# Performance work log

Measured on AMD Instinct MI355X. Metric: run time of the kernel, lower is better.

## Reference

```python
import jax, jax.numpy as jnp
import numpy as np

D_MODEL = 2048
N_HEADS = 16
N_KV = 4
D_HEAD = D_MODEL // N_HEADS  # 128
N_REP = N_HEADS // N_KV      # 4
ROPE_BASE = 1000000.0


def _rope_tables(T, d_head, dtype):
    # inv_freq = (1/base)^(2i/d) for i in [0, d/2)
    i = jnp.arange(d_head // 2, dtype=jnp.float32)
    inv_freq = (1.0 / ROPE_BASE) ** (2.0 * i / d_head)
    theta = jnp.arange(T, dtype=jnp.float32)[:, None] * inv_freq[None, :]  # [T, d/2]
    theta = jnp.concatenate([theta, theta], axis=-1)                        # [T, d]
    return jnp.sin(theta).astype(dtype), jnp.cos(theta).astype(dtype)


def _apply_rope(x, sin, cos):
    # x: [B, h, T, d]; sin/cos: [T, d]
    x1, x2 = jnp.split(x, 2, axis=-1)
    rot = jnp.concatenate([-x2, x1], axis=-1)
    return cos[None, None] * x + sin[None, None] * rot


def setup_inputs() -> dict:
    key = jax.random.key(0)
    ks = jax.random.split(key, 9)
    B, T = 2, 2048
    s_in = 1.0 / np.sqrt(D_MODEL)
    return {
        "x": jax.random.normal(ks[0], (B, T, D_MODEL), jnp.float32),
        "wq": jax.random.normal(ks[1], (D_MODEL, N_HEADS * D_HEAD), jnp.float32) * s_in,
        "bq": jax.random.normal(ks[2], (N_HEADS * D_HEAD,), jnp.float32) * 0.02,
        "wk": jax.random.normal(ks[3], (D_MODEL, N_KV * D_HEAD), jnp.float32) * s_in,
        "bk": jax.random.normal(ks[4], (N_KV * D_HEAD,), jnp.float32) * 0.02,
        "wv": jax.random.normal(ks[5], (D_MODEL, N_KV * D_HEAD), jnp.float32) * s_in,
        "bv": jax.random.normal(ks[6], (N_KV * D_HEAD,), jnp.float32) * 0.02,
        "wo": jax.random.normal(ks[7], (D_MODEL, D_MODEL), jnp.float32) * s_in,
    }


def reference(x, wq, bq, wk, bk, wv, bv, wo):
    B, T, C = x.shape
    sin, cos = _rope_tables(T, D_HEAD, x.dtype)

    q = (x @ wq + bq).reshape(B, T, N_HEADS, D_HEAD).transpose(0, 2, 1, 3)  # [B,H,T,d]
    k = (x @ wk + bk).reshape(B, T, N_KV, D_HEAD).transpose(0, 2, 1, 3)     # [B,KV,T,d]
    v = (x @ wv + bv).reshape(B, T, N_KV, D_HEAD).transpose(0, 2, 1, 3)     # [B,KV,T,d]

    q = _apply_rope(q, sin, cos)
    k = _apply_rope(k, sin, cos)

    # GQA: group query heads as [B, KV, rep, T, d] to broadcast against k/v
    qg = q.reshape(B, N_KV, N_REP, T, D_HEAD)
    scale = 1.0 / jnp.sqrt(jnp.asarray(D_HEAD, x.dtype))
    scores = jnp.einsum('bkrqd,bksd->bkrqs', qg, k) * scale  # [B,KV,rep,T,S]

    causal = jnp.tril(jnp.ones((T, T), dtype=bool))
    neg = jnp.asarray(jnp.finfo(x.dtype).min, x.dtype)
    scores = jnp.where(causal[None, None, None], scores, neg)
    p = jax.nn.softmax(scores, axis=-1)

    out = jnp.einsum('bkrqs,bksd->bkrqd', p, v)               # [B,KV,rep,T,d]
    out = out.reshape(B, N_HEADS, T, D_HEAD).transpose(0, 2, 1, 3).reshape(B, T, C)
    return out @ wo, k, v
```

## Files before the change

### kernel.cpp

```cpp
#include <hip/hip_runtime.h>
#include <hip/hip_bf16.h>
#include <math.h>

#define BB 2
#define TT 2048
#define DMODEL 2048
#define NH 16
#define NKV 4
#define DH 128
#define NQKV 3072
#define MM (BB*TT)

typedef unsigned short u16;
typedef unsigned int u32;

typedef __bf16 bf16x8 __attribute__((ext_vector_type(8)));
typedef __bf16 bf16x4 __attribute__((ext_vector_type(4)));
typedef short short4v __attribute__((ext_vector_type(4)));
typedef float f32x4 __attribute__((ext_vector_type(4)));

__device__ __forceinline__ u16 f2b(float f) {
  union { float f; u32 u; } v; v.f = f;
  u32 r = v.u + 0x7fffu + ((v.u >> 16) & 1u);
  return (u16)(r >> 16);
}
__device__ __forceinline__ float b2f(u16 h) {
  union { u32 u; float f; } v; v.u = ((u32)h) << 16;
  return v.f;
}
__device__ __forceinline__ u32 pack2bf(float x, float y) {
  union { float f; u32 u; } a, b; a.f = x; b.f = y;
  return ((a.u + 0x8000u) >> 16) | ((b.u + 0x8000u) & 0xffff0000u);
}

__device__ __forceinline__ void gload16(const void* g, void* l) {
  __builtin_amdgcn_global_load_lds(
      (const __attribute__((address_space(1))) unsigned int*)g,
      (__attribute__((address_space(3))) unsigned int*)l, 16, 0, 0);
}

__device__ __forceinline__ float fast_exp2(float x) {
#if __has_builtin(__builtin_amdgcn_exp2f)
  return __builtin_amdgcn_exp2f(x);
#else
  return __expf(x * 0.6931471805599453f);
#endif
}

__device__ __forceinline__ f32x4 mfma16(bf16x4 a, bf16x4 b, f32x4 c) {
#if __has_builtin(__builtin_amdgcn_mfma_f32_16x16x16bf16_1k)
  union { bf16x4 b; short4v s; } ua, ub;
  ua.b = a; ub.b = b;
  return __builtin_amdgcn_mfma_f32_16x16x16bf16_1k(ua.s, ub.s, c, 0, 0, 0);
#elif __has_builtin(__builtin_amdgcn_mfma_f32_16x16x16_bf16)
  return __builtin_amdgcn_mfma_f32_16x16x16_bf16(a, b, c, 0, 0, 0);
#else
  asm volatile("v_mfma_f32_16x16x16_bf16 %0, %1, %2, %0"
               : "+v"(c) : "v"(a), "v"(b));
  return c;
#endif
}

__global__ void cvt_x_kernel(const float* __restrict__ x, u16* __restrict__ xb, int n4) {
  int i = blockIdx.x * 256 + threadIdx.x;
  if (i < n4) {
    float4 v = ((const float4*)x)[i];
    u32 lo = (u32)f2b(v.x) | ((u32)f2b(v.y) << 16);
    u32 hi = (u32)f2b(v.z) | ((u32)f2b(v.w) << 16);
    uint2 r; r.x = lo; r.y = hi;
    ((uint2*)xb)[i] = r;
  }
}

__global__ void bias_cat_kernel(const float* __restrict__ bq, const float* __restrict__ bk,
                                const float* __restrict__ bv, float* __restrict__ bc) {
  int i = blockIdx.x * 256 + threadIdx.x;
  if (i < NQKV) bc[i] = (i < 2048) ? bq[i] : ((i < 2560) ? bk[i - 2048] : bv[i - 2560]);
}

__global__ void transpose_cvt_kernel(const float* __restrict__ src, u16* __restrict__ dst,
                                     int srcCols, int dstRowOff) {
  __shared__ u16 t[64][65];
  int c0 = blockIdx.x * 64, r0 = blockIdx.y * 64;
  int tid = threadIdx.x;
  for (int i = tid; i < 4096; i += 256) {
    int r = i >> 6, c = i & 63;
    t[r][c] = f2b(src[(size_t)(r0 + r) * srcCols + c0 + c]);
  }
  __syncthreads();
  for (int i = tid; i < 4096; i += 256) {
    int n = i >> 6, k = i & 63;
    dst[(size_t)(dstRowOff + c0 + n) * 2048 + r0 + k] = t[k][n];
  }
}

__global__ void vt_transpose_kernel(const u16* __restrict__ qkvb, u16* __restrict__ vt) {
  __shared__ u16 t[64][65];
  int bkv = blockIdx.z;
  int b  = bkv >> 2;
  int kv = bkv & 3;
  int d0 = blockIdx.y * 64;
  int t0 = blockIdx.x * 64;
  int tid = threadIdx.x;
  for (int i = tid; i < 4096; i += 256) {
    int r = i >> 6, c = i & 63;
    t[r][c] = qkvb[(size_t)(b * TT + t0 + r) * NQKV + 2560 + kv * DH + d0 + c];
  }
  __syncthreads();
  size_t tilebase = ((size_t)bkv * 32 + (t0 >> 6)) * 8192;
  for (int i = tid; i < 512; i += 256) {
    int dl = i & 63, chunk = i >> 6;
    int m = chunk >> 2, qd = chunk & 3;
    u16 tmp[8];
#pragma unroll
    for (int e = 0; e < 8; e++) {
      int srow = (2 * m + (e >> 2)) * 16 + qd * 4 + (e & 3);
      tmp[e] = t[srow][dl];
    }
    *(uint4*)&vt[tilebase + (size_t)(chunk * 128 + d0 + dl) * 8] = *(const uint4*)tmp;
  }
}

__global__ void rope_pack_kernel(const u16* __restrict__ qkvb, u16* __restrict__ qb,
                                 u16* __restrict__ kb, float* __restrict__ outK,
                                 float* __restrict__ outV) {
  __shared__ float sc_s[64], sc_c[64];
  int t = blockIdx.x, b = blockIdx.y;
  int tid = threadIdx.x;
  if (tid < 64) {
    float inv = exp2f(-(float)tid * 0.31143075889569023f);
    float th = (float)t * inv;
    sc_s[tid] = sinf(th);
    sc_c[tid] = cosf(th);
  }
  __syncthreads();
  const u16* row = qkvb + (size_t)(b * TT + t) * NQKV;
  const int rl = t & 63;
  const int tt = t >> 6;

  if (tid < 128) {
    int h = tid >> 3, oc = tid & 7;
    uint4 lo = *(const uint4*)&row[h * DH + oc * 8];
    uint4 hi = *(const uint4*)&row[h * DH + 64 + oc * 8];
    const u16* plo = (const u16*)&lo;
    const u16* phi = (const u16*)&hi;
    u16 y1[8], y2[8];
#pragma unroll
    for (int j = 0; j < 8; j++) {
      int d = oc * 8 + j;
      float x1 = b2f(plo[j]), x2 = b2f(phi[j]);
      float s = sc_s[d], c = sc_c[d];
      y1[j] = f2b(c * x1 - s * x2);
      y2[j] = f2b(c * x2 + s * x1);
    }
    size_t tb = ((size_t)(b * NH + h) * 32 + tt) * 8192;
    *(uint4*)&qb[tb + (size_t)((oc)     * 64 + rl) * 8] = *(const uint4*)y1;
    *(uint4*)&qb[tb + (size_t)((oc + 8) * 64 + rl) * 8] = *(const uint4*)y2;
  } else if (tid < 160) {
    int id = tid - 128;
    int kv = id >> 3, oc = id & 7;
    uint4 lo = *(const uint4*)&row[2048 + kv * DH + oc * 8];
    uint4 hi = *(const uint4*)&row[2048 + kv * DH + 64 + oc * 8];
    const u16* plo = (const u16*)&lo;
    const u16* phi = (const u16*)&hi;
    u16 y1[8], y2[8];
    float f1[8], f2v[8];
#pragma unroll
    for (int j = 0; j < 8; j++) {
      int d = oc * 8 + j;
      float x1 = b2f(plo[j]), x2 = b2f(phi[j]);
      float s = sc_s[d], c = sc_c[d];
      f1[j] = c * x1 - s * x2;
      f2v[j] = c * x2 + s * x1;
      y1[j] = f2b(f1[j]);
      y2[j] = f2b(f2v[j]);
    }
    size_t tb = ((size_t)(b * NKV + kv) * 32 + tt) * 8192;
    *(uint4*)&kb[tb + (size_t)((oc)     * 64 + rl) * 8] = *(const uint4*)y1;
    *(uint4*)&kb[tb + (size_t)((oc + 8) * 64 + rl) * 8] = *(const uint4*)y2;
    size_t base = ((size_t)(b * NKV + kv) * TT + t) * DH + oc * 8;
    *(float4*)&outK[base]     = *(const float4*)&f1[0];
    *(float4*)&outK[base + 4] = *(const float4*)&f1[4];
    *(float4*)&outK[base + 64]     = *(const float4*)&f2v[0];
    *(float4*)&outK[base + 64 + 4] = *(const float4*)&f2v[4];
  } else if (tid < 224) {
    int id = tid - 160;
    int kv = id >> 4, oc = id & 15;
    uint4 v = *(const uint4*)&row[2560 + kv * DH + oc * 8];
    const u16* pv = (const u16*)&v;
    float f[8];
#pragma unroll
    for (int j = 0; j < 8; j++) f[j] = b2f(pv[j]);
    size_t base = ((size_t)(b * NKV + kv) * TT + t) * DH + oc * 8;
    *(float4*)&outV[base]     = *(const float4*)&f[0];
    *(float4*)&outV[base + 4] = *(const float4*)&f[4];
  }
}

template <int BIAS, int OUTF32>
__global__ __launch_bounds__(256, 3) void gemm_kernel(
    const u16* __restrict__ A, const u16* __restrict__ Bt,
    const float* __restrict__ bias, void* __restrict__ Cout,
    int M, int N, int K) {
  __shared__ u16 lA[128 * 32];
  __shared__ u16 lB[128 * 32];
  const int tid  = threadIdx.x;
  const int lane = tid & 63;
  const int wave = tid >> 6;
  const int quad = lane >> 4;
  const int l16  = lane & 15;
  const int m0 = blockIdx.y * 128;
  const int n0 = blockIdx.x * 128;
  const int wrow = (wave >> 1) * 64;
  const int wcol = (wave & 1) * 64;

  f32x4 acc[4][4];
  const f32x4 zero = {0.f, 0.f, 0.f, 0.f};
#pragma unroll
  for (int i = 0; i < 4; i++)
#pragma unroll
    for (int j = 0; j < 4; j++) acc[i][j] = zero;

  const int srow = tid >> 2;
  const int scol = (tid & 3) * 8;

  const u16* ga = A  + (size_t)(m0 + srow) * K + scol;
  const u16* gb = Bt + (size_t)(n0 + srow) * K + scol;

  for (int k0 = 0; k0 < K; k0 += 32) {
    gload16(ga + k0,                  &lA[tid * 8]);
    gload16(ga + k0 + (size_t)64 * K, &lA[2048 + tid * 8]);
    gload16(gb + k0,                  &lB[tid * 8]);
    gload16(gb + k0 + (size_t)64 * K, &lB[2048 + tid * 8]);
    __syncthreads();
    bf16x8 af[4], bf[4];
#pragma unroll
    for (int mi = 0; mi < 4; mi++)
      af[mi] = *(const bf16x8*)&lA[(wrow + mi * 16 + l16) * 32 + quad * 8];
#pragma unroll
    for (int ni = 0; ni < 4; ni++)
      bf[ni] = *(const bf16x8*)&lB[(wcol + ni * 16 + l16) * 32 + quad * 8];
#pragma unroll
    for (int mi = 0; mi < 4; mi++)
#pragma unroll
      for (int ni = 0; ni < 4; ni++)
        acc[mi][ni] = __builtin_amdgcn_mfma_f32_16x16x32_bf16(af[mi], bf[ni], acc[mi][ni], 0, 0, 0);
    __syncthreads();
  }

#pragma unroll
  for (int ni = 0; ni < 4; ni++) {
    int gcol = n0 + wcol + ni * 16 + l16;
    float bval = BIAS ? bias[gcol] : 0.0f;
#pragma unroll
    for (int mi = 0; mi < 4; mi++) {
#pragma unroll
      for (int r = 0; r < 4; r++) {
        int grow = m0 + wrow + mi * 16 + quad * 4 + r;
        float v = acc[mi][ni][r] + bval;
        if (OUTF32) ((float*)Cout)[(size_t)grow * N + gcol] = v;
        else        ((u16*)Cout)[(size_t)grow * N + gcol]   = f2b(v);
      }
    }
  }
}

__global__ __launch_bounds__(256, 2) void attn_kernel(
    const u16* __restrict__ Qt, const u16* __restrict__ Kt,
    const u16* __restrict__ Vt, u16* __restrict__ Ob) {
  __shared__ u16 sm[24576];
  u16* vbuf = sm + 16384;

  const int bh = blockIdx.y;
  const int b = bh >> 4, h = bh & 15, kv = h >> 2;
  const int tid = threadIdx.x;
  const int lane = tid & 63;
  const int wave = tid >> 6;
  const int quad = lane >> 4;
  const int l16 = lane & 15;

  const u16* qbase = Qt + (size_t)(b * NH + h) * 32 * 8192;
  const u16* kbase = Kt + (size_t)(b * NKV + kv) * 32 * 8192;
  const u16* vbase = Vt + (size_t)(b * NKV + kv) * 32 * 8192;

  const f32x4 zero = {0.f, 0.f, 0.f, 0.f};
  const float SC2 = 0.08838834764831845f * 1.4426950408889634f;
  const float NEGINF = -__builtin_inff();

  int par = 0;

#pragma unroll
  for (int p = 0; p < 4; p++)
    gload16(kbase + p * 2048 + tid * 8, sm + p * 2048 + tid * 8);

  for (int half = 0; half < 2; ++half) {
    const int qt = half ? (31 - (int)blockIdx.x) : (int)blockIdx.x;
    const int q0 = qt * 64;
    const u16* qtile = qbase + (size_t)qt * 8192;
    const int qrel = wave * 16 + l16;

    bf16x8 qf[4];
#pragma unroll
    for (int kc = 0; kc < 4; kc++)
      qf[kc] = *(const bf16x8*)&qtile[(size_t)((kc * 4 + quad) * 64 + qrel) * 8];

    float mrow = NEGINF, lrow = 0.f;
    f32x4 o[8];
#pragma unroll
    for (int d = 0; d < 8; d++) o[d] = zero;

    for (int kt = 0; kt <= qt; ++kt) {
      u16* kb_c = sm + par * 8192;
      u16* kb_n = sm + (par ^ 1) * 8192;
      const int ktn = (kt < qt) ? kt + 1 : 0;
      const u16* vsrc = vbase + (size_t)kt * 8192;
      const u16* knxt = kbase + (size_t)ktn * 8192;
#pragma unroll
      for (int p = 0; p < 4; p++)
        gload16(vsrc + p * 2048 + tid * 8, vbuf + p * 2048 + tid * 8);
#pragma unroll
      for (int p = 0; p < 4; p++)
        gload16(knxt + p * 2048 + tid * 8, kb_n + p * 2048 + tid * 8);
      asm volatile("s_waitcnt vmcnt(8)\n\ts_barrier" ::: "memory");

      f32x4 sv[4];
#pragma unroll
      for (int mt = 0; mt < 4; mt++) sv[mt] = zero;
#pragma unroll
      for (int kc = 0; kc < 4; kc++) {
#pragma unroll
        for (int mt = 0; mt < 4; mt++) {
          bf16x8 kf = *(const bf16x8*)&kb_c[(size_t)((kc * 4 + quad) * 64 + mt * 16 + l16) * 8];
          sv[mt] = __builtin_amdgcn_mfma_f32_16x16x32_bf16(kf, qf[kc], sv[mt], 0, 0, 0);
        }
      }

      if (kt == qt) {
#pragma unroll
        for (int mt = 0; mt < 4; mt++) {
#pragma unroll
          for (int r = 0; r < 4; r++) {
            int srel = mt * 16 + quad * 4 + r;
            if (srel > qrel) sv[mt][r] = NEGINF;
          }
        }
      }
      float mraw = NEGINF;
#pragma unroll
      for (int mt = 0; mt < 4; mt++)
#pragma unroll
        for (int r = 0; r < 4; r++) mraw = fmaxf(mraw, sv[mt][r]);
      mraw = fmaxf(mraw, __shfl_xor(mraw, 16));
      mraw = fmaxf(mraw, __shfl_xor(mraw, 32));

      float mnew = fmaxf(mrow, mraw);
      float alpha = fast_exp2((mrow - mnew) * SC2);
      mrow = mnew;
      float msc = mnew * SC2;
      float lsum = 0.f;
#pragma unroll
      for (int mt = 0; mt < 4; mt++) {
#pragma unroll
        for (int r = 0; r < 4; r++) {
          float p = fast_exp2(__builtin_fmaf(sv[mt][r], SC2, -msc));
          sv[mt][r] = p;
          lsum += p;
        }
      }
      lsum += __shfl_xor(lsum, 16);
      lsum += __shfl_xor(lsum, 32);
      lrow = lrow * alpha + lsum;
      bf16x4 pb[4];
#pragma unroll
      for (int mt = 0; mt < 4; mt++) {
        union { u32 u[2]; bf16x4 v; } pu;
        pu.u[0] = pack2bf(sv[mt][0], sv[mt][1]);
        pu.u[1] = pack2bf(sv[mt][2], sv[mt][3]);
        pb[mt] = pu.v;
      }
#pragma unroll
      for (int dt = 0; dt < 8; dt++) {
        o[dt][0] *= alpha; o[dt][1] *= alpha; o[dt][2] *= alpha; o[dt][3] *= alpha;
      }

      asm volatile("s_waitcnt vmcnt(4)\n\ts_barrier" ::: "memory");
#pragma unroll
      for (int m = 0; m < 2; m++) {
#pragma unroll
        for (int dt = 0; dt < 8; dt++) {
          bf16x8 vf = *(const bf16x8*)&vbuf[(size_t)(((m * 4 + quad) * 128) + dt * 16 + l16) * 8];
          bf16x4 vlo = __builtin_shufflevector(vf, vf, 0, 1, 2, 3);
          bf16x4 vhi = __builtin_shufflevector(vf, vf, 4, 5, 6, 7);
          o[dt] = mfma16(vlo, pb[2 * m],     o[dt]);
          o[dt] = mfma16(vhi, pb[2 * m + 1], o[dt]);
        }
      }
      asm volatile("s_barrier" ::: "memory");
      par ^= 1;
    }

    float inv = 1.0f / lrow;
    int t = q0 + qrel;
    size_t rowbase = (size_t)(b * TT + t) * DMODEL + h * DH;
#pragma unroll
    for (int dt = 0; dt < 8; dt++) {
      uint2 w;
      w.x = pack2bf(o[dt][0] * inv, o[dt][1] * inv);
      w.y = pack2bf(o[dt][2] * inv, o[dt][3] * inv);
      *(uint2*)&Ob[rowbase + dt * 16 + quad * 4] = w;
    }
  }
}

extern "C" void kernel_launch(void* const* d_in, const int* in_sizes, int n_in,
                              void* d_out, int out_size, void* d_ws, size_t ws_size,
                              hipStream_t stream) {
  (void)in_sizes; (void)n_in; (void)out_size; (void)ws_size;
  const float* x  = (const float*)d_in[0];
  const float* wq = (const float*)d_in[1];
  const float* bq = (const float*)d_in[2];
  const float* wk = (const float*)d_in[3];
  const float* bk = (const float*)d_in[4];
  const float* wv = (const float*)d_in[5];
  const float* bv = (const float*)d_in[6];
  const float* wo = (const float*)d_in[7];
  float* out = (float*)d_out;

  char* ws = (char*)d_ws;
  u16*   xb    = (u16*)(ws);
  u16*   wqkvT = (u16*)(ws + 16777216);
  u16*   woT   = (u16*)(ws + 29360128);
  float* bcat  = (float*)(ws + 37748736);
  u16*   qkvb  = (u16*)(ws + 37761024);
  u16*   qb    = (u16*)(ws + 62926848);
  u16*   kb    = (u16*)(ws + 79704064);
  u16*   vt    = (u16*)(ws + 83898368);
  u16*   ob    = (u16*)(ws + 88092672);

  float* outK = out + (size_t)BB * TT * DMODEL;
  float* outV = outK + (size_t)BB * NKV * TT * DH;

  cvt_x_kernel<<<8192, 256, 0, stream>>>(x, xb, (BB * TT * DMODEL) / 4);
  bias_cat_kernel<<<12, 256, 0, stream>>>(bq, bk, bv, bcat);
  transpose_cvt_kernel<<<dim3(32, 32), 256, 0, stream>>>(wq, wqkvT, 2048, 0);
  transpose_cvt_kernel<<<dim3(8, 32),  256, 0, stream>>>(wk, wqkvT, 512, 2048);
  transpose_cvt_kernel<<<dim3(8, 32),  256, 0, stream>>>(wv, wqkvT, 512, 2560);
  transpose_cvt_kernel<<<dim3(32, 32), 256, 0, stream>>>(wo, woT, 2048, 0);

  gemm_kernel<1, 0><<<dim3(NQKV / 128, MM / 128), 256, 0, stream>>>(
      xb, wqkvT, bcat, qkvb, MM, NQKV, DMODEL);

  rope_pack_kernel<<<dim3(TT, BB), 256, 0, stream>>>(qkvb, qb, kb, outK, outV);
  vt_transpose_kernel<<<dim3(TT / 64, DH / 64, BB * NKV), 256, 0, stream>>>(qkvb, vt);

  attn_kernel<<<dim3(16, BB * NH), 256, 0, stream>>>(qb, kb, vt, ob);

  gemm_kernel<0, 1><<<dim3(DMODEL / 128, MM / 128), 256, 0, stream>>>(
      ob, woT, nullptr, out, MM, DMODEL, DMODEL);
}
```

Before: 342.0 us.

## Fuse bias, RoPE and K/V packing into QKV GEMM epilogue; double-buffer GEMM loads

The separate bias-concat, RoPE/pack and V-transpose kernels are folded into the QKV GEMM epilogue. The epilogue stages the bf16 tile in shared memory, then writes the attention-ready Q/K/V layouts plus the fp32 K/V outputs, so the intermediate qkvb buffer never round-trips through global memory. Both GEMMs now double-buffer their shared-memory loads with a prefetch of the next k-slice, and RoPE sin/cos come from a precomputed table. In attention, the row-sum cross-lane reduction is deferred to the end instead of running every iteration. The costs are larger shared memory per block and heavier epilogue work that may strain registers.

```diff
diff --git a/kernel.cpp b/kernel.cpp
--- a/kernel.cpp
+++ b/kernel.cpp
@@ -72,10 +72,13 @@
   }
 }
 
-__global__ void bias_cat_kernel(const float* __restrict__ bq, const float* __restrict__ bk,
-                                const float* __restrict__ bv, float* __restrict__ bc) {
+__global__ void rope_table_kernel(float2* __restrict__ tab) {
   int i = blockIdx.x * 256 + threadIdx.x;
-  if (i < NQKV) bc[i] = (i < 2048) ? bq[i] : ((i < 2560) ? bk[i - 2048] : bv[i - 2560]);
+  int t = i >> 6, d = i & 63;
+  float inv = exp2f(-(float)d * 0.31143075889569023f);
+  float th = (float)t * inv;
+  float2 cs; cs.x = cosf(th); cs.y = sinf(th);
+  tab[i] = cs;
 }
 
 __global__ void transpose_cvt_kernel(const float* __restrict__ src, u16* __restrict__ dst,
@@ -94,116 +97,165 @@
   }
 }
 
-__global__ void vt_transpose_kernel(const u16* __restrict__ qkvb, u16* __restrict__ vt) {
-  __shared__ u16 t[64][65];
-  int bkv = blockIdx.z;
-  int b  = bkv >> 2;
-  int kv = bkv & 3;
-  int d0 = blockIdx.y * 64;
-  int t0 = blockIdx.x * 64;
-  int tid = threadIdx.x;
-  for (int i = tid; i < 4096; i += 256) {
-    int r = i >> 6, c = i & 63;
-    t[r][c] = qkvb[(size_t)(b * TT + t0 + r) * NQKV + 2560 + kv * DH + d0 + c];
+__global__ __launch_bounds__(256, 3) void gemm_qkv_kernel(
+    const u16* __restrict__ A, const u16* __restrict__ Bt,
+    const float* __restrict__ bq, const float* __restrict__ bk,
+    const float* __restrict__ bv, const float2* __restrict__ rtab,
+    u16* __restrict__ qb, u16* __restrict__ kb, u16* __restrict__ vt,
+    float* __restrict__ outK, float* __restrict__ outV) {
+  __shared__ __align__(16) u16 sm[16384];
+  const int K = DMODEL;
+  const int tid  = threadIdx.x;
+  const int lane = tid & 63;
+  const int wave = tid >> 6;
+  const int quad = lane >> 4;
+  const int l16  = lane & 15;
+  const int m0 = blockIdx.y * 128;
+  const int n0 = blockIdx.x * 128;
+  const int nh = blockIdx.x;
+  const int wrow = (wave >> 1) * 64;
+  const int wcol = (wave & 1) * 64;
+
+  f32x4 acc[4][4];
+  const f32x4 zero = {0.f, 0.f, 0.f, 0.f};
+#pragma unroll
+  for (int i = 0; i < 4; i++)
+#pragma unroll
+    for (int j = 0; j < 4; j++) acc[i][j] = zero;
+
+  const int srow = tid >> 2;
+  const int scol = (tid & 3) * 8;
+  const u16* ga = A  + (size_t)(m0 + srow) * K + scol;
+  const u16* gb = Bt + (size_t)(n0 + srow) * K + scol;
+
+  gload16(ga,                  &sm[tid * 8]);
+  gload16(ga + (size_t)64 * K, &sm[2048 + tid * 8]);
+  gload16(gb,                  &sm[4096 + tid * 8]);
+  gload16(gb + (size_t)64 * K, &sm[6144 + tid * 8]);
+
+  for (int k0 = 0; k0 < K; k0 += 32) {
+    const int p = (k0 >> 5) & 1;
+    const int kn = (k0 + 32 == K) ? 0 : k0 + 32;
+    u16* nb = &sm[(p ^ 1) * 8192];
+    gload16(ga + kn,                  nb + tid * 8);
+    gload16(ga + kn + (size_t)64 * K, nb + 2048 + tid * 8);
+    gload16(gb + kn,                  nb + 4096 + tid * 8);
+    gload16(gb + kn + (size_t)64 * K, nb + 6144 + tid * 8);
+    asm volatile("s_waitcnt vmcnt(4)\n\ts_barrier" ::: "memory");
+    const u16* cb = &sm[p * 8192];
+    bf16x8 af[4], bf[4];
+#pragma unroll
+    for (int mi = 0; mi < 4; mi++)
+      af[mi] = *(const bf16x8*)&cb[(wrow + mi * 16 + l16) * 32 + quad * 8];
+#pragma unroll
+    for (int ni = 0; ni < 4; ni++)
+      bf[ni] = *(const bf16x8*)&cb[4096 + (wcol + ni * 16 + l16) * 32 + quad * 8];
+    asm volatile("s_waitcnt lgkmcnt(0)\n\ts_barrier" ::: "memory");
+#pragma unroll
+    for (int mi = 0; mi < 4; mi++)
+#pragma unroll
+      for (int ni = 0; ni < 4; ni++)
+        acc[mi][ni] = __builtin_amdgcn_mfma_f32_16x16x32_bf16(af[mi], bf[ni], acc[mi][ni], 0, 0, 0);
+  }
+
+  asm volatile("s_waitcnt vmcnt(0)\n\ts_barrier" ::: "memory");
+
+#pragma unroll
+  for (int ni = 0; ni < 4; ni++) {
+    int col = wcol + ni * 16 + l16;
+    int gcol = n0 + col;
+    float bval = (nh < 16) ? bq[gcol] : ((nh < 20) ? bk[gcol - 2048] : bv[gcol - 2560]);
+#pragma unroll
+    for (int mi = 0; mi < 4; mi++) {
+#pragma unroll
+      for (int r = 0; r < 4; r++) {
+        int row = wrow + mi * 16 + quad * 4 + r;
+        sm[row * 128 + col] = f2b(acc[mi][ni][r] + bval);
+      }
+    }
   }
   __syncthreads();
-  size_t tilebase = ((size_t)bkv * 32 + (t0 >> 6)) * 8192;
-  for (int i = tid; i < 512; i += 256) {
-    int dl = i & 63, chunk = i >> 6;
-    int m = chunk >> 2, qd = chunk & 3;
-    u16 tmp[8];
-#pragma unroll
-    for (int e = 0; e < 8; e++) {
-      int srow = (2 * m + (e >> 2)) * 16 + qd * 4 + (e & 3);
-      tmp[e] = t[srow][dl];
-    }
-    *(uint4*)&vt[tilebase + (size_t)(chunk * 128 + d0 + dl) * 8] = *(const uint4*)tmp;
-  }
-}
-
-__global__ void rope_pack_kernel(const u16* __restrict__ qkvb, u16* __restrict__ qb,
-                                 u16* __restrict__ kb, float* __restrict__ outK,
-                                 float* __restrict__ outV) {
-  __shared__ float sc_s[64], sc_c[64];
-  int t = blockIdx.x, b = blockIdx.y;
-  int tid = threadIdx.x;
-  if (tid < 64) {
-    float inv = exp2f(-(float)tid * 0.31143075889569023f);
-    float th = (float)t * inv;
-    sc_s[tid] = sinf(th);
-    sc_c[tid] = cosf(th);
-  }
-  __syncthreads();
-  const u16* row = qkvb + (size_t)(b * TT + t) * NQKV;
-  const int rl = t & 63;
-  const int tt = t >> 6;
-
-  if (tid < 128) {
-    int h = tid >> 3, oc = tid & 7;
-    uint4 lo = *(const uint4*)&row[h * DH + oc * 8];
-    uint4 hi = *(const uint4*)&row[h * DH + 64 + oc * 8];
-    const u16* plo = (const u16*)&lo;
-    const u16* phi = (const u16*)&hi;
-    u16 y1[8], y2[8];
-#pragma unroll
-    for (int j = 0; j < 8; j++) {
-      int d = oc * 8 + j;
-      float x1 = b2f(plo[j]), x2 = b2f(phi[j]);
-      float s = sc_s[d], c = sc_c[d];
-      y1[j] = f2b(c * x1 - s * x2);
-      y2[j] = f2b(c * x2 + s * x1);
-    }
-    size_t tb = ((size_t)(b * NH + h) * 32 + tt) * 8192;
-    *(uint4*)&qb[tb + (size_t)((oc)     * 64 + rl) * 8] = *(const uint4*)y1;
-    *(uint4*)&qb[tb + (size_t)((oc + 8) * 64 + rl) * 8] = *(const uint4*)y2;
-  } else if (tid < 160) {
-    int id = tid - 128;
-    int kv = id >> 3, oc = id & 7;
-    uint4 lo = *(const uint4*)&row[2048 + kv * DH + oc * 8];
-    uint4 hi = *(const uint4*)&row[2048 + kv * DH + 64 + oc * 8];
-    const u16* plo = (const u16*)&lo;
-    const u16* phi = (const u16*)&hi;
-    u16 y1[8], y2[8];
-    float f1[8], f2v[8];
-#pragma unroll
-    for (int j = 0; j < 8; j++) {
-      int d = oc * 8 + j;
-      float x1 = b2f(plo[j]), x2 = b2f(phi[j]);
-      float s = sc_s[d], c = sc_c[d];
-      f1[j] = c * x1 - s * x2;
-      f2v[j] = c * x2 + s * x1;
-      y1[j] = f2b(f1[j]);
-      y2[j] = f2b(f2v[j]);
-    }
-    size_t tb = ((size_t)(b * NKV + kv) * 32 + tt) * 8192;
-    *(uint4*)&kb[tb + (size_t)((oc)     * 64 + rl) * 8] = *(const uint4*)y1;
-    *(uint4*)&kb[tb + (size_t)((oc + 8) * 64 + rl) * 8] = *(const uint4*)y2;
-    size_t base = ((size_t)(b * NKV + kv) * TT + t) * DH + oc * 8;
-    *(float4*)&outK[base]     = *(const float4*)&f1[0];
-    *(float4*)&outK[base + 4] = *(const float4*)&f1[4];
-    *(float4*)&outK[base + 64]     = *(const float4*)&f2v[0];
-    *(float4*)&outK[base + 64 + 4] = *(const float4*)&f2v[4];
-  } else if (tid < 224) {
-    int id = tid - 160;
-    int kv = id >> 4, oc = id & 15;
-    uint4 v = *(const uint4*)&row[2560 + kv * DH + oc * 8];
-    const u16* pv = (const u16*)&v;
-    float f[8];
-#pragma unroll
-    for (int j = 0; j < 8; j++) f[j] = b2f(pv[j]);
-    size_t base = ((size_t)(b * NKV + kv) * TT + t) * DH + oc * 8;
-    *(float4*)&outV[base]     = *(const float4*)&f[0];
-    *(float4*)&outV[base + 4] = *(const float4*)&f[4];
-  }
-}
-
-template <int BIAS, int OUTF32>
-__global__ __launch_bounds__(256, 3) void gemm_kernel(
+
+  const int bidx = m0 >> 11;
+  const int trow0 = m0 & 2047;
+
+  if (nh < 20) {
+    const int isQ = (nh < 16);
+    const int hh = isQ ? nh : (nh - 16);
+#pragma unroll
+    for (int it = 0; it < 4; it++) {
+      int id = tid + it * 256;
+      int row = id >> 3, oc = id & 7;
+      int t = trow0 + row;
+      int rl = t & 63, ttile = t >> 6;
+      uint4 lo = *(const uint4*)&sm[row * 128 + oc * 8];
+      uint4 hi = *(const uint4*)&sm[row * 128 + 64 + oc * 8];
+      const u16* plo = (const u16*)&lo;
+      const u16* phi = (const u16*)&hi;
+      u16 y1[8], y2[8];
+      float f1[8], f2v[8];
+#pragma unroll
+      for (int j = 0; j < 8; j++) {
+        float2 cs = rtab[(t << 6) + oc * 8 + j];
+        float x1 = b2f(plo[j]), x2 = b2f(phi[j]);
+        f1[j]  = cs.x * x1 - cs.y * x2;
+        f2v[j] = cs.x * x2 + cs.y * x1;
+        y1[j] = f2b(f1[j]);
+        y2[j] = f2b(f2v[j]);
+      }
+      if (isQ) {
+        size_t tb = ((size_t)(bidx * NH + hh) * 32 + ttile) * 8192;
+        *(uint4*)&qb[tb + (size_t)((oc)     * 64 + rl) * 8] = *(const uint4*)y1;
+        *(uint4*)&qb[tb + (size_t)((oc + 8) * 64 + rl) * 8] = *(const uint4*)y2;
+      } else {
+        size_t tb = ((size_t)(bidx * NKV + hh) * 32 + ttile) * 8192;
+        *(uint4*)&kb[tb + (size_t)((oc)     * 64 + rl) * 8] = *(const uint4*)y1;
+        *(uint4*)&kb[tb + (size_t)((oc + 8) * 64 + rl) * 8] = *(const uint4*)y2;
+        size_t base = ((size_t)(bidx * NKV + hh) * TT + t) * DH + oc * 8;
+        *(float4*)&outK[base]          = *(const float4*)&f1[0];
+        *(float4*)&outK[base + 4]      = *(const float4*)&f1[4];
+        *(float4*)&outK[base + 64]     = *(const float4*)&f2v[0];
+        *(float4*)&outK[base + 64 + 4] = *(const float4*)&f2v[4];
+      }
+    }
+  } else {
+    const int kvh = nh - 20;
+#pragma unroll
+    for (int it = 0; it < 8; it++) {
+      int id = tid + it * 256;
+      int row = id >> 4, oc = id & 15;
+      uint4 v = *(const uint4*)&sm[row * 128 + oc * 8];
+      const u16* pv = (const u16*)&v;
+      float f[8];
+#pragma unroll
+      for (int j = 0; j < 8; j++) f[j] = b2f(pv[j]);
+      size_t base = ((size_t)(bidx * NKV + kvh) * TT + trow0 + row) * DH + oc * 8;
+      *(float4*)&outV[base]     = *(const float4*)&f[0];
+      *(float4*)&outV[base + 4] = *(const float4*)&f[4];
+    }
+#pragma unroll
+    for (int it = 0; it < 8; it++) {
+      int id = tid + it * 256;
+      int tile = id >> 10, rem = id & 1023;
+      int chunk = rem >> 7, dl = rem & 127;
+      int m = chunk >> 2, qd = chunk & 3;
+      u16 tmp[8];
+#pragma unroll
+      for (int e = 0; e < 8; e++) {
+        int srw = (2 * m + (e >> 2)) * 16 + qd * 4 + (e & 3);
+        tmp[e] = sm[(tile * 64 + srw) * 128 + dl];
+      }
+      int tt = (trow0 >> 6) + tile;
+      size_t tilebase = ((size_t)(bidx * NKV + kvh) * 32 + tt) * 8192;
+      *(uint4*)&vt[tilebase + (size_t)(chunk * 128 + dl) * 8] = *(const uint4*)tmp;
+    }
+  }
+}
+
+__global__ __launch_bounds__(256, 3) void gemm_out_kernel(
     const u16* __restrict__ A, const u16* __restrict__ Bt,
-    const float* __restrict__ bias, void* __restrict__ Cout,
-    int M, int N, int K) {
-  __shared__ u16 lA[128 * 32];
-  __shared__ u16 lB[128 * 32];
+    float* __restrict__ Cout, int M, int N, int K) {
+  __shared__ __align__(16) u16 sm[16384];
   const int tid  = threadIdx.x;
   const int lane = tid & 63;
   const int wave = tid >> 6;
@@ -223,43 +275,49 @@
 
   const int srow = tid >> 2;
   const int scol = (tid & 3) * 8;
-
   const u16* ga = A  + (size_t)(m0 + srow) * K + scol;
   const u16* gb = Bt + (size_t)(n0 + srow) * K + scol;
 
+  gload16(ga,                  &sm[tid * 8]);
+  gload16(ga + (size_t)64 * K, &sm[2048 + tid * 8]);
+  gload16(gb,                  &sm[4096 + tid * 8]);
+  gload16(gb + (size_t)64 * K, &sm[6144 + tid * 8]);
+
   for (int k0 = 0; k0 < K; k0 += 32) {
-    gload16(ga + k0,                  &lA[tid * 8]);
-    gload16(ga + k0 + (size_t)64 * K, &lA[2048 + tid * 8]);
-    gload16(gb + k0,                  &lB[tid * 8]);
-    gload16(gb + k0 + (size_t)64 * K, &lB[2048 + tid * 8]);
-    __syncthreads();
+    const int p = (k0 >> 5) & 1;
+    const int kn = (k0 + 32 == K) ? 0 : k0 + 32;
+    u16* nb = &sm[(p ^ 1) * 8192];
+    gload16(ga + kn,                  nb + tid * 8);
+    gload16(ga + kn + (size_t)64 * K, nb + 2048 + tid * 8);
+    gload16(gb + kn,                  nb + 4096 + tid * 8);
+    gload16(gb + kn + (size_t)64 * K, nb + 6144 + tid * 8);
+    asm volatile("s_waitcnt vmcnt(4)\n\ts_barrier" ::: "memory");
+    const u16* cb = &sm[p * 8192];
     bf16x8 af[4], bf[4];
 #pragma unroll
     for (int mi = 0; mi < 4; mi++)
-      af[mi] = *(const bf16x8*)&lA[(wrow + mi * 16 + l16) * 32 + quad * 8];
+      af[mi] = *(const bf16x8*)&cb[(wrow + mi * 16 + l16) * 32 + quad * 8];
 #pragma unroll
     for (int ni = 0; ni < 4; ni++)
-      bf[ni] = *(const bf16x8*)&lB[(wcol + ni * 16 + l16) * 32 + quad * 8];
+      bf[ni] = *(const bf16x8*)&cb[4096 + (wcol + ni * 16 + l16) * 32 + quad * 8];
+    asm volatile("s_waitcnt lgkmcnt(0)\n\ts_barrier" ::: "memory");
 #pragma unroll
     for (int mi = 0; mi < 4; mi++)
 #pragma unroll
       for (int ni = 0; ni < 4; ni++)
         acc[mi][ni] = __builtin_amdgcn_mfma_f32_16x16x32_bf16(af[mi], bf[ni], acc[mi][ni], 0, 0, 0);
-    __syncthreads();
-  }
+  }
+  asm volatile("s_waitcnt vmcnt(0)" ::: "memory");
 
 #pragma unroll
   for (int ni = 0; ni < 4; ni++) {
     int gcol = n0 + wcol + ni * 16 + l16;
-    float bval = BIAS ? bias[gcol] : 0.0f;
 #pragma unroll
     for (int mi = 0; mi < 4; mi++) {
 #pragma unroll
       for (int r = 0; r < 4; r++) {
         int grow = m0 + wrow + mi * 16 + quad * 4 + r;
-        float v = acc[mi][ni][r] + bval;
-        if (OUTF32) ((float*)Cout)[(size_t)grow * N + gcol] = v;
-        else        ((u16*)Cout)[(size_t)grow * N + gcol]   = f2b(v);
+        Cout[(size_t)grow * N + gcol] = acc[mi][ni][r];
       }
     }
   }
@@ -268,7 +326,7 @@
 __global__ __launch_bounds__(256, 2) void attn_kernel(
     const u16* __restrict__ Qt, const u16* __restrict__ Kt,
     const u16* __restrict__ Vt, u16* __restrict__ Ob) {
-  __shared__ u16 sm[24576];
+  __shared__ __align__(16) u16 sm[24576];
   u16* vbuf = sm + 16384;
 
   const int bh = blockIdx.y;
@@ -337,13 +395,12 @@
 
       if (kt == qt) {
 #pragma unroll
-        for (int mt = 0; mt < 4; mt++) {
+        for (int mt = 0; mt < 4; mt++)
 #pragma unroll
           for (int r = 0; r < 4; r++) {
             int srel = mt * 16 + quad * 4 + r;
             if (srel > qrel) sv[mt][r] = NEGINF;
           }
-        }
       }
       float mraw = NEGINF;
 #pragma unroll
@@ -367,8 +424,6 @@
           lsum += p;
         }
       }
-      lsum += __shfl_xor(lsum, 16);
-      lsum += __shfl_xor(lsum, 32);
       lrow = lrow * alpha + lsum;
       bf16x4 pb[4];
 #pragma unroll
@@ -399,6 +454,8 @@
       par ^= 1;
     }
 
+    lrow += __shfl_xor(lrow, 16);
+    lrow += __shfl_xor(lrow, 32);
     float inv = 1.0f / lrow;
     int t = q0 + qrel;
     size_t rowbase = (size_t)(b * TT + t) * DMODEL + h * DH;
@@ -410,6 +467,7 @@
       *(uint2*)&Ob[rowbase + dt * 16 + quad * 4] = w;
     }
   }
+  asm volatile("s_waitcnt vmcnt(0)" ::: "memory");
 }
 
 extern "C" void kernel_launch(void* const* d_in, const int* in_sizes, int n_in,
@@ -427,34 +485,30 @@
   float* out = (float*)d_out;
 
   char* ws = (char*)d_ws;
-  u16*   xb    = (u16*)(ws);
-  u16*   wqkvT = (u16*)(ws + 16777216);
-  u16*   woT   = (u16*)(ws + 29360128);
-  float* bcat  = (float*)(ws + 37748736);
-  u16*   qkvb  = (u16*)(ws + 37761024);
-  u16*   qb    = (u16*)(ws + 62926848);
-  u16*   kb    = (u16*)(ws + 79704064);
-  u16*   vt    = (u16*)(ws + 83898368);
-  u16*   ob    = (u16*)(ws + 88092672);
+  u16*    xb    = (u16*)(ws);
+  u16*    wqkvT = (u16*)(ws + 16777216);
+  u16*    woT   = (u16*)(ws + 29360128);
+  float2* rtab  = (float2*)(ws + 37748736);
+  u16*    qb    = (u16*)(ws + 38797312);
+  u16*    kb    = (u16*)(ws + 55574528);
+  u16*    vt    = (u16*)(ws + 59768832);
+  u16*    ob    = (u16*)(ws + 63963136);
 
   float* outK = out + (size_t)BB * TT * DMODEL;
   float* outV = outK + (size_t)BB * NKV * TT * DH;
 
   cvt_x_kernel<<<8192, 256, 0, stream>>>(x, xb, (BB * TT * DMODEL) / 4);
-  bias_cat_kernel<<<12, 256, 0, stream>>>(bq, bk, bv, bcat);
+  rope_table_kernel<<<512, 256, 0, stream>>>(rtab);
   transpose_cvt_kernel<<<dim3(32, 32), 256, 0, stream>>>(wq, wqkvT, 2048, 0);
   transpose_cvt_kernel<<<dim3(8, 32),  256, 0, stream>>>(wk, wqkvT, 512, 2048);
   transpose_cvt_kernel<<<dim3(8, 32),  256, 0, stream>>>(wv, wqkvT, 512, 2560);
   transpose_cvt_kernel<<<dim3(32, 32), 256, 0, stream>>>(wo, woT, 2048, 0);
 
-  gemm_kernel<1, 0><<<dim3(NQKV / 128, MM / 128), 256, 0, stream>>>(
-      xb, wqkvT, bcat, qkvb, MM, NQKV, DMODEL);
-
-  rope_pack_kernel<<<dim3(TT, BB), 256, 0, stream>>>(qkvb, qb, kb, outK, outV);
-  vt_transpose_kernel<<<dim3(TT / 64, DH / 64, BB * NKV), 256, 0, stream>>>(qkvb, vt);
+  gemm_qkv_kernel<<<dim3(NQKV / 128, MM / 128), 256, 0, stream>>>(
+      xb, wqkvT, bq, bk, bv, rtab, qb, kb, vt, outK, outV);
 
   attn_kernel<<<dim3(16, BB * NH), 256, 0, stream>>>(qb, kb, vt, ob);
 
-  gemm_kernel<0, 1><<<dim3(DMODEL / 128, MM / 128), 256, 0, stream>>>(
-      ob, woT, nullptr, out, MM, DMODEL, DMODEL);
-}
+  gemm_out_kernel<<<dim3(DMODEL / 128, MM / 128), 256, 0, stream>>>(
+      ob, woT, out, MM, DMODEL, DMODEL);
+}
```

New measurement: 315.4 us. 7.8% less time.
